# Performance work log

Hardware: AMD Instinct MI355X
Metric: run time of the kernel (lower is better)

The kernel has to match this reference:

```python
import jax, jax.numpy as jnp
import numpy as np

B, Q, K, D, H = 2, 1024, 4096, 1024, 16
DH = D // H
LN_EPS = 1e-5


def setup_inputs() -> dict:
    key = jax.random.key(0)
    ks = jax.random.split(key, 10)
    queries = jax.random.normal(ks[0], (B, Q, D), jnp.float32)
    keys = jax.random.normal(ks[1], (B, K, D), jnp.float32)
    values = jax.random.normal(ks[2], (B, K, D), jnp.float32)
    # 128 words of 8 query tokens each: boundaries 0,8,...,1024 (sorted, unique)
    word_boundaries = jnp.arange(0, Q + 1, 8, dtype=jnp.int32)  # [129]
    # monotone map from query positions to char/key positions in [0, K]
    char_boundaries = jnp.sort(jax.random.randint(ks[3], (Q,), 0, K + 1, dtype=jnp.int32))
    s = 0.02
    ln_gamma = jnp.ones((D,), jnp.float32)
    ln_beta = jnp.zeros((D,), jnp.float32)
    in_proj_w = jax.random.normal(ks[4], (3 * D, D), jnp.float32) * s
    in_proj_b = jnp.zeros((3 * D,), jnp.float32)
    out_w = jax.random.normal(ks[5], (D, D), jnp.float32) * s
    out_b = jnp.zeros((D,), jnp.float32)
    return dict(queries=queries, keys=keys, values=values,
                word_boundaries=word_boundaries, char_boundaries=char_boundaries,
                ln_gamma=ln_gamma, ln_beta=ln_beta,
                in_proj_w=in_proj_w, in_proj_b=in_proj_b,
                out_w=out_w, out_b=out_b)


def char_aware_mask(wb, cb, q_len, k_len):
    """Vectorized version of the per-word python loop.
    Float mask of 0/1 (PyTorch ADDS a float attn_mask to the scores)."""
    ws, we = wb[:-1], wb[1:]                     # word start/end in query coords [nW]
    nW = ws.shape[0]
    cs = cb[ws]                                  # char span start per word
    ce = cb[we - 1]                              # char span end per word
    q = jnp.arange(q_len)
    i = jnp.clip(jnp.searchsorted(wb, q, side='right') - 1, 0, nW - 1)  # word id per query row
    valid = (q >= ws[i]) & (q < we[i])           # rows actually written by the loop
    j = jnp.arange(k_len)[None, :]               # [1, K]
    in_char = (j >= cs[i][:, None]) & (j < ce[i][:, None])
    # prev word: keys [wb[i-1], wb[i]) (query-coord indices used on key axis, as in source)
    ps = ws[jnp.maximum(i - 1, 0)]
    in_prev = (i > 0)[:, None] & (j >= ps[:, None]) & (j < ws[i][:, None])
    # next word: keys [wb[i+1], wb[i+2])
    ns = we[i]
    ne = wb[jnp.minimum(i + 2, nW)]
    in_next = (i < nW - 1)[:, None] & (j >= ns[:, None]) & (j < ne[:, None])
    return (valid[:, None] & (in_char | in_prev | in_next)).astype(jnp.float32)


def reference(queries, keys, values, word_boundaries, char_boundaries,
              ln_gamma, ln_beta, in_proj_w, in_proj_b, out_w, out_b):
    b, q_len, d = queries.shape
    k_len = keys.shape[1]
    mask = char_aware_mask(word_boundaries, char_boundaries, q_len, k_len)  # [Q, K]
    # LayerNorm(queries)
    mu = jnp.mean(queries, axis=-1, keepdims=True)
    var = jnp.var(queries, axis=-1, keepdims=True)
    x = (queries - mu) * jax.lax.rsqrt(var + LN_EPS) * ln_gamma + ln_beta
    # MultiheadAttention(x, keys, values, attn_mask=mask) -- float mask added to logits
    wq, wk, wv = jnp.split(in_proj_w, 3, axis=0)
    bq, bk, bv = jnp.split(in_proj_b, 3)
    qh = (x @ wq.T + bq).reshape(b, q_len, H, DH)
    kh = (keys @ wk.T + bk).reshape(b, k_len, H, DH)
    vh = (values @ wv.T + bv).reshape(b, k_len, H, DH)
    scale = 1.0 / jnp.sqrt(jnp.asarray(DH, queries.dtype))
    scores = jnp.einsum('bqhd,bkhd->bhqk', qh * scale, kh) + mask[None, None]
    attn = jax.nn.softmax(scores, axis=-1)
    ctx = jnp.einsum('bhqk,bkhd->bqhd', attn, vh).reshape(b, q_len, d)
    out = ctx @ out_w.T + out_b
    # residual; dropout is identity at inference
    return queries + out
```

## Files before the change

### kernel.cpp

```cpp
#include <hip/hip_runtime.h>
#include <hip/hip_bf16.h>


typedef __attribute__((ext_vector_type(8))) short bf16x8;
typedef __attribute__((ext_vector_type(4))) float f32x4;
typedef __attribute__((ext_vector_type(16))) float f32x16;

#define L2E 1.44269504088896341f
#define CSCALE (0.125f * L2E)
#define NSPLIT 4

__device__ __forceinline__ short f2bf(float f) {
  __hip_bfloat16 h = __float2bfloat16(f);
  return reinterpret_cast<short&>(h);
}

__device__ __forceinline__ unsigned cvtpk(float a, float b) {
  unsigned r;
  asm("v_cvt_pk_bf16_f32 %0, %1, %2" : "=v"(r) : "v"(a), "v"(b));
  return r;
}

__device__ __forceinline__ float fexp2(float x) {
#if __has_builtin(__builtin_amdgcn_exp2f)
  return __builtin_amdgcn_exp2f(x);
#else
  float r;
  asm("v_exp_f32 %0, %1" : "=v"(r) : "v"(x));
  return r;
#endif
}

__device__ __forceinline__ void halfswap(unsigned a, unsigned b, unsigned& x, unsigned& y) {
#if __has_builtin(__builtin_amdgcn_permlane32_swap)
  auto r = __builtin_amdgcn_permlane32_swap(a, b, false, false);
  x = (unsigned)r[0];
  y = (unsigned)r[1];
#else
  unsigned ca = (unsigned)__shfl_xor((int)a, 32);
  unsigned cb = (unsigned)__shfl_xor((int)b, 32);
  bool h = ((threadIdx.x & 63) >> 5) != 0;
  x = h ? cb : a;
  y = h ? b : ca;
#endif
}

__device__ __forceinline__ void gload16(const void* g, void* l) {
  __builtin_amdgcn_global_load_lds(
      (const __attribute__((address_space(1))) void*)g,
      (__attribute__((address_space(3))) void*)l, 16, 0, 0);
}

template <int N>
__device__ __forceinline__ void phase_end() {
  __builtin_amdgcn_sched_barrier(0);
  if constexpr (N == 8)
    asm volatile("s_waitcnt vmcnt(8)" ::: "memory");
  else if constexpr (N == 6)
    asm volatile("s_waitcnt vmcnt(6)" ::: "memory");
  else if constexpr (N == 5)
    asm volatile("s_waitcnt vmcnt(5)" ::: "memory");
  else if constexpr (N == 4)
    asm volatile("s_waitcnt vmcnt(4)" ::: "memory");
  else if constexpr (N == 2)
    asm volatile("s_waitcnt vmcnt(2)" ::: "memory");
  else
    asm volatile("s_waitcnt vmcnt(0)" ::: "memory");
  __builtin_amdgcn_s_barrier();
  __builtin_amdgcn_sched_barrier(0);
}

__device__ __forceinline__ void wait_lgkm0() {
  __builtin_amdgcn_sched_barrier(0);
  asm volatile("s_waitcnt lgkmcnt(0)" ::: "memory");
  __builtin_amdgcn_sched_barrier(0);
}

__global__ __launch_bounds__(256) void prep_kernel(const float* __restrict__ w,
                                                   const float* __restrict__ o,
                                                   short* __restrict__ dw,
                                                   short* __restrict__ dof,
                                                   const float* __restrict__ x,
                                                   const float* __restrict__ gamma,
                                                   const float* __restrict__ beta,
                                                   short* __restrict__ xout,
                                                   const int* __restrict__ wb,
                                                   const int* __restrict__ cb,
                                                   int* __restrict__ iv,
                                                   const float* __restrict__ keys,
                                                   const float* __restrict__ values,
                                                   short* __restrict__ kbf,
                                                   short* __restrict__ vbf) {
  const int blk = blockIdx.x;
  const int t = threadIdx.x;
  if (blk < 4096) {
    long i = ((long)blk * 256 + t) * 4;
    const float* s;
    short* d;
    if (i < 3145728) { s = w + i; d = dw + i; }
    else { s = o + (i - 3145728); d = dof + (i - 3145728); }
    float4 xv = *(const float4*)s;
    uint2 r;
    r.x = cvtpk(xv.x, xv.y);
    r.y = cvtpk(xv.z, xv.w);
    *(uint2*)d = r;
  } else if (blk < 6144) {
    const int row = blk - 4096;
    float4 v = ((const float4*)(x + (size_t)row * 1024))[t];
    float s = v.x + v.y + v.z + v.w;
    float ss = v.x * v.x + v.y * v.y + v.z * v.z + v.w * v.w;
#pragma unroll
    for (int d = 32; d; d >>= 1) { s += __shfl_xor(s, d); ss += __shfl_xor(ss, d); }
    __shared__ float red[8];
    int wv2 = t >> 6, lane = t & 63;
    if (lane == 0) { red[wv2] = s; red[4 + wv2] = ss; }
    __syncthreads();
    s = red[0] + red[1] + red[2] + red[3];
    ss = red[4] + red[5] + red[6] + red[7];
    float mean = s * (1.0f / 1024.0f);
    float var = ss * (1.0f / 1024.0f) - mean * mean;
    float rstd = rsqrtf(var + 1e-5f);
    float4 g = ((const float4*)gamma)[t];
    float4 b = ((const float4*)beta)[t];
    uint2 oo;
    oo.x = cvtpk((v.x - mean) * rstd * g.x + b.x, (v.y - mean) * rstd * g.y + b.y);
    oo.y = cvtpk((v.z - mean) * rstd * g.z + b.z, (v.w - mean) * rstd * g.w + b.w);
    ((uint2*)(xout + (size_t)row * 1024))[t] = oo;
  } else if (blk < 6148) {
    int q = (blk - 6144) * 256 + t;
    if (q >= 1024) return;
    int cnt = 0;
    for (int k = 0; k < 129; ++k) cnt += (wb[k] <= q) ? 1 : 0;
    int i = cnt - 1;
    i = i < 0 ? 0 : (i > 127 ? 127 : i);
    bool valid = (q >= wb[i]) && (q < wb[i + 1]);
    int cs = 0, ce = 0, pl = 0, ph = 0, nl = 0, nh = 0;
    if (valid) {
      cs = cb[wb[i]];
      ce = cb[wb[i + 1] - 1];
      if (i > 0) { pl = wb[i - 1]; ph = wb[i]; }
      if (i < 127) { nl = wb[i + 1]; nh = wb[(i + 2 <= 128) ? i + 2 : 128]; }
    }
    int* p = iv + q * 8;
    p[0] = cs; p[1] = ce; p[2] = pl; p[3] = ph; p[4] = nl; p[5] = nh; p[6] = 0; p[7] = 0;
  } else {
    long i = ((long)(blk - 6148) * 256 + t) * 4;
    const float* s;
    short* d;
    if (i < 8388608) { s = keys + i; d = kbf + i; }
    else { s = values + (i - 8388608); d = vbf + (i - 8388608); }
    float4 xv = *(const float4*)s;
    uint2 r;
    r.x = cvtpk(xv.x, xv.y);
    r.y = cvtpk(xv.z, xv.w);
    *(uint2*)d = r;
  }
}

__device__ __forceinline__ unsigned inrange3(int key, const int* p) {
  bool m = (key >= p[0] && key < p[1]) || (key >= p[2] && key < p[3]) ||
           (key >= p[4] && key < p[5]);
  return m ? 1u : 0u;
}

__global__ __launch_bounds__(256) void mask_frag_kernel(const int* __restrict__ iv,
                                                        uint4* __restrict__ pmf) {
  int idx = blockIdx.x * 256 + threadIdx.x;
  int lane = idx & 63;
  int wg = (idx >> 6) & 31;
  int t = idx >> 11;
  int l31 = lane & 31, hi = lane >> 5;
  uint4 o = {0u, 0u, 0u, 0u};
  if (!hi) {
    int key0 = t * 64 + l31, key1 = key0 + 32;
    const int* p0 = iv + (wg * 32 + 0) * 8;
    const int* p1 = iv + (wg * 32 + 8) * 8;
    const int* p2 = iv + (wg * 32 + 16) * 8;
    const int* p3 = iv + (wg * 32 + 24) * 8;
    unsigned b0 = inrange3(key0, p0), b1 = inrange3(key0, p1);
    unsigned b2 = inrange3(key0, p2), b3 = inrange3(key0, p3);
    o.x = (b0 | (b1 << 16)) * 0x3F80u;
    o.y = (b2 | (b3 << 16)) * 0x3F80u;
    b0 = inrange3(key1, p0); b1 = inrange3(key1, p1);
    b2 = inrange3(key1, p2); b3 = inrange3(key1, p3);
    o.z = (b0 | (b1 << 16)) * 0x3F80u;
    o.w = (b2 | (b3 << 16)) * 0x3F80u;
  }
  pmf[idx] = o;
}

__device__ __forceinline__ void kv256_body(short* lds, const short* __restrict__ Agl,
                                           const short* __restrict__ Bgl,
                                           const float* __restrict__ bias,
                                           short* __restrict__ Cout, int mode,
                                           int bx, int by) {
  const int tid = (int)threadIdx.x;
  const int lane = tid & 63;
  const int w = tid >> 6;
  const int wm = w >> 2, wn = w & 3;
  const int l16 = lane & 15, lhi = lane >> 4;
  const int gc8 = (lane & 7) ^ (lane >> 3);
  const int lr = lane >> 3;
  const int rsw = (l16 & 7) << 4;
  const int m0 = bx * 256, n0 = by * 256;

  f32x4 acc[8][4];
#pragma unroll
  for (int i = 0; i < 8; ++i)
#pragma unroll
    for (int j = 0; j < 4; ++j) acc[i][j] = f32x4{0.f, 0.f, 0.f, 0.f};

  auto SU = [&](int k, int unit) {
    const int k0 = k * 64;
    short* base = lds + (k & 1) * 32768;
#pragma unroll
    for (int j = 0; j < 2; ++j) {
      int i = w * 2 + j;
      int ch;
      bool isA;
      if (unit == 1)      { ch = (i < 8) ? i : i + 8;       isA = true; }
      else if (unit == 4) { ch = 8 + ((i < 8) ? i : i + 8); isA = true; }
      else if (unit == 2) { ch = (i >> 2) * 8 + (i & 3);    isA = false; }
      else                { ch = 4 + (i >> 2) * 8 + (i & 3); isA = false; }
      const short* g = isA ? (Agl + (size_t)(m0 + ch * 8 + lr) * 1024 + k0 + gc8 * 8)
                           : (Bgl + (size_t)(n0 + ch * 8 + lr) * 1024 + k0 + gc8 * 8);
      gload16(g, base + (isA ? 0 : 16384) + ch * 512);
    }
  };

  bf16x8 af[4][2], b0[2][2], b1[2][2];
  auto LDA = [&](int bsel, int qm) {
    const char* cA = (const char*)(lds + bsel * 32768);
#pragma unroll
    for (int mt = 0; mt < 4; ++mt)
#pragma unroll
      for (int kk = 0; kk < 2; ++kk) {
        int row = wm * 128 + qm * 64 + mt * 16 + l16;
        af[mt][kk] = *(const bf16x8*)(cA + row * 128 + ((kk * 64 + lhi * 16) ^ rsw));
      }
  };
  auto LDB = [&](int bsel, int qn, bf16x8 (&bf)[2][2]) {
    const char* cB = (const char*)(lds + bsel * 32768) + 32768;
#pragma unroll
    for (int nt = 0; nt < 2; ++nt)
#pragma unroll
      for (int kk = 0; kk < 2; ++kk) {
        int row = wn * 64 + qn * 32 + nt * 16 + l16;
        bf[nt][kk] = *(const bf16x8*)(cB + row * 128 + ((kk * 64 + lhi * 16) ^ rsw));
      }
  };
  auto MM = [&](int qm, int qn, bf16x8 (&bf)[2][2]) {
    __builtin_amdgcn_s_setprio(1);
#pragma unroll
    for (int kk = 0; kk < 2; ++kk)
#pragma unroll
      for (int mt = 0; mt < 4; ++mt)
#pragma unroll
        for (int nt = 0; nt < 2; ++nt)
          acc[qm * 4 + mt][qn * 2 + nt] = __builtin_amdgcn_mfma_f32_16x16x32_bf16(
              af[mt][kk], bf[nt][kk], acc[qm * 4 + mt][qn * 2 + nt], 0, 0, 0);
    __builtin_amdgcn_s_setprio(0);
  };

  SU(0, 1); SU(0, 2); SU(0, 3); SU(0, 4);
  SU(1, 1); SU(1, 2);
  phase_end<8>();

#pragma unroll 2
  for (int k = 0; k < 14; ++k) {
    const int bs = k & 1;
    LDA(bs, 0); LDB(bs, 0, b0); SU(k + 1, 3);
    wait_lgkm0(); MM(0, 0, b0); phase_end<8>();
    LDB(bs, 1, b1); SU(k + 1, 4);
    wait_lgkm0(); MM(0, 1, b1); phase_end<8>();
    LDA(bs, 1); SU(k + 2, 1);
    wait_lgkm0(); MM(1, 0, b0); phase_end<8>();
    SU(k + 2, 2);
    MM(1, 1, b1); phase_end<8>();
  }
  {
    LDA(0, 0); LDB(0, 0, b0); SU(15, 3);
    wait_lgkm0(); MM(0, 0, b0); phase_end<8>();
    LDB(0, 1, b1); SU(15, 4);
    wait_lgkm0(); MM(0, 1, b1); phase_end<8>();
    LDA(0, 1);
    wait_lgkm0(); MM(1, 0, b0); phase_end<8>();
    MM(1, 1, b1); phase_end<4>();
  }
  {
    LDA(1, 0); LDB(1, 0, b0);
    wait_lgkm0(); MM(0, 0, b0); phase_end<2>();
    LDB(1, 1, b1);
    wait_lgkm0(); MM(0, 1, b1); phase_end<0>();
    LDA(1, 1);
    wait_lgkm0(); MM(1, 0, b0);
    MM(1, 1, b1);
  }

#pragma unroll
  for (int mt = 0; mt < 8; ++mt)
#pragma unroll
    for (int nt = 0; nt < 4; ++nt) {
      int n = n0 + wn * 64 + nt * 16 + l16;
#pragma unroll
      for (int r = 0; r < 4; ++r) {
        int m = m0 + wm * 128 + mt * 16 + lhi * 4 + r;
        float v = acc[mt][nt][r];
        if (mode == 0) {
          int bb = m >> 12, key = m & 4095;
          int hh = n >> 6, dhl = n & 63;
          Cout[((size_t)((bb * 16 + hh) * 4096 + key)) * 64 + dhl] = f2bf(v + bias[n]);
        } else {
          int bb = n >> 12, key = n & 4095;
          Cout[((size_t)(bb * 1024 + m)) * 4096 + key] = f2bf(v + bias[m]);
        }
      }
    }
}

__device__ __forceinline__ void gemmQO_body(short* lA, short* lB,
                                            const short* __restrict__ A,
                                            const short* __restrict__ W,
                                            const float* __restrict__ bias,
                                            const float* __restrict__ resid,
                                            void* __restrict__ Cout, int mode,
                                            float scale, int bxi, int byi) {
  const int lane = threadIdx.x & 63;
  const int w = threadIdx.x >> 6;
  const int m0 = bxi * 64;
  const int n0 = byi * 128;
  const int wm = w >> 2, wn = w & 3;
  const int l16 = lane & 15, lhi = lane >> 4;

  const int gc8 = (lane & 7) ^ (lane >> 3);
  const int lr = lane >> 3;
  const int rsw = (l16 & 7) << 4;

  f32x4 zero = {0.f, 0.f, 0.f, 0.f};
  f32x4 acc[2][2];
#pragma unroll
  for (int i = 0; i < 2; ++i)
#pragma unroll
    for (int j = 0; j < 2; ++j) acc[i][j] = zero;

  for (int k0 = 0; k0 < 1024; k0 += 64) {
    __syncthreads();
#pragma unroll
    for (int j = 0; j < 3; ++j) {
      int c = w * 3 + j;
      if (c < 8)
        gload16(A + (size_t)(m0 + c * 8 + lr) * 1024 + k0 + gc8 * 8, &lA[c * 512]);
      else
        gload16(W + (size_t)(n0 + (c - 8) * 8 + lr) * 1024 + k0 + gc8 * 8,
                &lB[(c - 8) * 512]);
    }
    __syncthreads();
    bf16x8 af[2][2], bfr[2][2];
#pragma unroll
    for (int mt = 0; mt < 2; ++mt)
#pragma unroll
      for (int kk = 0; kk < 2; ++kk)
        af[mt][kk] = *(const bf16x8*)((const char*)lA + (wm * 32 + mt * 16 + l16) * 128 +
                                      ((kk * 64 + lhi * 16) ^ rsw));
#pragma unroll
    for (int nt = 0; nt < 2; ++nt)
#pragma unroll
      for (int kk = 0; kk < 2; ++kk)
        bfr[nt][kk] = *(const bf16x8*)((const char*)lB + (wn * 32 + nt * 16 + l16) * 128 +
                                       ((kk * 64 + lhi * 16) ^ rsw));
#pragma unroll
    for (int kk = 0; kk < 2; ++kk)
#pragma unroll
      for (int mt = 0; mt < 2; ++mt)
#pragma unroll
        for (int nt = 0; nt < 2; ++nt)
          acc[mt][nt] = __builtin_amdgcn_mfma_f32_16x16x32_bf16(af[mt][kk], bfr[nt][kk],
                                                                acc[mt][nt], 0, 0, 0);
  }

#pragma unroll
  for (int mt = 0; mt < 2; ++mt)
#pragma unroll
    for (int nt = 0; nt < 2; ++nt) {
      int col = n0 + wn * 32 + nt * 16 + l16;
      float bs = bias[col];
#pragma unroll
      for (int r = 0; r < 4; ++r) {
        int row = m0 + wm * 32 + mt * 16 + lhi * 4 + r;
        float v = acc[mt][nt][r] + bs;
        if (mode == 0) {
          ((short*)Cout)[(size_t)row * 1024 + col] = f2bf(v * scale);
        } else {
          size_t idx = (size_t)row * 1024 + col;
          ((float*)Cout)[idx] = v + resid[idx];
        }
      }
    }
}

__global__ __launch_bounds__(512, 2) void megaGemm_kernel(const short* __restrict__ kbf,
                                                          const short* __restrict__ wk,
                                                          const float* __restrict__ kbias,
                                                          const short* __restrict__ wv,
                                                          const short* __restrict__ vbf,
                                                          const float* __restrict__ vbias,
                                                          short* __restrict__ khp,
                                                          short* __restrict__ vhT,
                                                          const short* __restrict__ xb,
                                                          const short* __restrict__ wq,
                                                          const float* __restrict__ qbias,
                                                          short* __restrict__ qhb) {
  __shared__ __attribute__((aligned(16))) short lds[65536];
  int id = blockIdx.x;
  if (id < 128) {
    kv256_body(lds, kbf, wk, kbias, khp, 0, id & 31, id >> 5);
  } else if (id < 256) {
    int i2 = id & 127;
    kv256_body(lds, wv, vbf, vbias, vhT, 1, i2 >> 5, i2 & 31);
  } else {
    int i2 = id - 256;
    gemmQO_body(lds, lds + 4096, xb, wq, qbias, nullptr, qhb, 0, CSCALE, i2 & 31, i2 >> 5);
  }
}

__global__ __launch_bounds__(512, 4) void gemmQO_kernel(const short* __restrict__ A,
                                                        const short* __restrict__ W,
                                                        const float* __restrict__ bias,
                                                        const float* __restrict__ resid,
                                                        void* __restrict__ Cout, int mode,
                                                        float scale) {
  __shared__ __attribute__((aligned(16))) short lA[4096];
  __shared__ __attribute__((aligned(16))) short lB[8192];
  gemmQO_body(lA, lB, A, W, bias, resid, Cout, mode, scale, blockIdx.x, blockIdx.y);
}

__global__ __launch_bounds__(256) void attn11_kernel(const short* __restrict__ qh,
                                                     const short* __restrict__ khp,
                                                     const short* __restrict__ vtp,
                                                     const uint4* __restrict__ pmf,
                                                     short* __restrict__ pacc,
                                                     float* __restrict__ pml) {
  const int tid = threadIdx.x;
  const int lane = tid & 63;
  const int w = tid >> 6;
  const int l31 = lane & 31;
  const int hi = lane >> 5;
  const int id = blockIdx.x;
  const int qb = id >> 7;
  const int g = id & 127;
  const int bh = g >> 2;
  const int ks = g & 3;
  const int b = bh >> 4, h = bh & 15;

  __shared__ __attribute__((aligned(16))) short sK[2][4096];
  __shared__ __attribute__((aligned(16))) short sV[2][4096];

  const int wq0 = qb * 128 + w * 32;
  const int qrow = wq0 + l31;
  bf16x8 qf0, qf1, qf2, qf3;
  {
    const short* qp = qh + ((size_t)(b * 1024 + qrow)) * 1024 + h * 64 + hi * 8;
    qf0 = *(const bf16x8*)(qp);
    qf1 = *(const bf16x8*)(qp + 16);
    qf2 = *(const bf16x8*)(qp + 32);
    qf3 = *(const bf16x8*)(qp + 48);
  }

  bf16x8 bmv;
  {
    union { unsigned u[4]; bf16x8 v; } t;
    t.u[0] = t.u[1] = t.u[2] = t.u[3] = 0;
    int lj = l31 >> 3;
    unsigned val = 0x3FB9u << (16 * (lj & 1));
    if (!hi) t.u[lj >> 1] = val;
    bmv = t.v;
  }

  f32x16 fzero;
#pragma unroll
  for (int i = 0; i < 16; ++i) fzero[i] = 0.f;

  const int kchunk = ks * 1024;
  const int sub = (lane & 7) ^ (lane >> 3);
  const int r8 = lane >> 3;
  const size_t kbase_g = ((size_t)bh * 4096 + kchunk) * 64;
  const size_t vbase_g = ((size_t)bh * 64) * 4096 + (size_t)kchunk;
  const uint4* pmfp = pmf + ((size_t)(ks * 16) * 32 + qb * 4 + w) * 64 + lane;

  f32x16 acc0, acc1;
#pragma unroll
  for (int i = 0; i < 16; ++i) { acc0[i] = 0.f; acc1[i] = 0.f; }
  float rs = 0.f;

  const int koff_swz = (lane & 7) << 4;

  auto STAGE = [&](int buf, int t) {
    int kt = t * 64;
#pragma unroll
    for (int q2 = 0; q2 < 2; ++q2) {
      int ch = w * 2 + q2;
      gload16(khp + kbase_g + (size_t)(kt + ch * 8 + r8) * 64 + sub * 8,
              (short*)sK[buf] + ch * 512);
      gload16(vtp + vbase_g + (size_t)(ch * 8 + r8) * 4096 + kt + sub * 8,
              (short*)sV[buf] + ch * 512);
    }
  };

  auto HALF = [&](int buf, unsigned mlo, unsigned mhi, int rowb, bf16x8& paA, bf16x8& paB) {
    bf16x8 am;
    {
      union { unsigned u[4]; bf16x8 v; } f;
      f.u[0] = mlo; f.u[1] = mhi; f.u[2] = 0; f.u[3] = 0;
      am = f.v;
    }
    __builtin_amdgcn_s_setprio(1);
    f32x16 ss = __builtin_amdgcn_mfma_f32_32x32x16_bf16(am, bmv, fzero, 0, 0, 0);
#pragma unroll
    for (int c = 0; c < 4; ++c) {
      int off = (c * 32 + hi * 16) ^ koff_swz;
      bf16x8 k0 = *(const bf16x8*)((const char*)sK[buf] + (rowb + l31) * 128 + off);
      bf16x8 qc = (c == 0) ? qf0 : (c == 1) ? qf1 : (c == 2) ? qf2 : qf3;
      ss = __builtin_amdgcn_mfma_f32_32x32x16_bf16(k0, qc, ss, 0, 0, 0);
    }
    __builtin_amdgcn_s_setprio(0);
#pragma unroll
    for (int r = 0; r < 16; ++r) ss[r] = fexp2(ss[r]);
    {
      float t0 = ss[0] + ss[1], t1 = ss[2] + ss[3], t2 = ss[4] + ss[5], t3 = ss[6] + ss[7];
      float t4 = ss[8] + ss[9], t5 = ss[10] + ss[11], t6 = ss[12] + ss[13],
            t7 = ss[14] + ss[15];
      rs += ((t0 + t1) + (t2 + t3)) + ((t4 + t5) + (t6 + t7));
    }
    unsigned a01 = cvtpk(ss[0], ss[1]), a23 = cvtpk(ss[2], ss[3]);
    unsigned a45 = cvtpk(ss[4], ss[5]), a67 = cvtpk(ss[6], ss[7]);
    unsigned a89 = cvtpk(ss[8], ss[9]), aAB = cvtpk(ss[10], ss[11]);
    unsigned aCD = cvtpk(ss[12], ss[13]), aEF = cvtpk(ss[14], ss[15]);
    union { unsigned u[4]; bf16x8 v; } f;
    halfswap(a01, a45, f.u[0], f.u[2]);
    halfswap(a23, a67, f.u[1], f.u[3]);
    paA = f.v;
    halfswap(a89, aCD, f.u[0], f.u[2]);
    halfswap(aAB, aEF, f.u[1], f.u[3]);
    paB = f.v;
  };

  uint4 mf_cur = pmfp[0];
  uint4 mf_next = mf_cur;
  STAGE(0, 0);
  __syncthreads();
  int buf = 0;

  for (int t = 0; t < 16; ++t) {
    if (t < 15) {
      STAGE(buf ^ 1, t + 1);
      mf_next = pmfp[(size_t)(t + 1) * 2048];
    }

    bf16x8 pa0, pa1, pa2, pa3;
    HALF(buf, mf_cur.x, mf_cur.y, 0, pa0, pa1);
    HALF(buf, mf_cur.z, mf_cur.w, 32, pa2, pa3);

    __builtin_amdgcn_s_setprio(1);
#pragma unroll
    for (int kb16 = 0; kb16 < 4; ++kb16) {
      int off = (kb16 * 32 + hi * 16) ^ koff_swz;
      bf16x8 v0 = *(const bf16x8*)((const char*)sV[buf] + l31 * 128 + off);
      bf16x8 v1 = *(const bf16x8*)((const char*)sV[buf] + (32 + l31) * 128 + off);
      bf16x8 pa = (kb16 == 0) ? pa0 : (kb16 == 1) ? pa1 : (kb16 == 2) ? pa2 : pa3;
      acc0 = __builtin_amdgcn_mfma_f32_32x32x16_bf16(pa, v0, acc0, 0, 0, 0);
      acc1 = __builtin_amdgcn_mfma_f32_32x32x16_bf16(pa, v1, acc1, 0, 0, 0);
    }
    __builtin_amdgcn_s_setprio(0);
    __syncthreads();
    buf ^= 1;
    mf_cur = mf_next;
  }

  short* paccp = pacc + (((size_t)ks * 32 + bh) * 1024) * 64;
#pragma unroll
  for (int r = 0; r < 16; r += 2) {
    int q0 = wq0 + ((r & 3) + 8 * (r >> 2)) + 4 * hi;
    int q1 = wq0 + (((r + 1) & 3) + 8 * ((r + 1) >> 2)) + 4 * hi;
    unsigned u0 = cvtpk(acc0[r], acc0[r + 1]);
    unsigned u1 = cvtpk(acc1[r], acc1[r + 1]);
    paccp[(size_t)q0 * 64 + l31] = (short)(u0 & 0xffffu);
    paccp[(size_t)q1 * 64 + l31] = (short)(u0 >> 16);
    paccp[(size_t)q0 * 64 + 32 + l31] = (short)(u1 & 0xffffu);
    paccp[(size_t)q1 * 64 + 32 + l31] = (short)(u1 >> 16);
  }
  rs += __shfl_xor(rs, 32);
  if (hi == 0) {
    float* mlp = pml + ((size_t)ks * 32 + bh) * 1024;
    mlp[wq0 + l31] = rs;
  }
}

__global__ __launch_bounds__(256) void combine_kernel(const short* __restrict__ pacc,
                                                      const float* __restrict__ pml,
                                                      short* __restrict__ ctx) {
  int idx = blockIdx.x * 256 + threadIdx.x;
  int dh4 = idx & 15;
  int row = idx >> 4;
  int bh = row >> 10, q = row & 1023;
  float L = 0.f, o0 = 0.f, o1 = 0.f, o2 = 0.f, o3 = 0.f;
#pragma unroll
  for (int k = 0; k < NSPLIT; ++k) {
    L += pml[((size_t)k * 32 + bh) * 1024 + q];
    uint2 u = *(const uint2*)&pacc[(((size_t)k * 32 + bh) * 1024 + q) * 64 + dh4 * 4];
    unsigned a = u.x, b2 = u.y;
    unsigned t0 = a << 16, t1 = a & 0xffff0000u, t2 = b2 << 16, t3 = b2 & 0xffff0000u;
    o0 += reinterpret_cast<float&>(t0);
    o1 += reinterpret_cast<float&>(t1);
    o2 += reinterpret_cast<float&>(t2);
    o3 += reinterpret_cast<float&>(t3);
  }
  float inv = 1.0f / L;
  uint2 st;
  st.x = cvtpk(o0 * inv, o1 * inv);
  st.y = cvtpk(o2 * inv, o3 * inv);
  int b = bh >> 4, h = bh & 15;
  *(uint2*)&ctx[((size_t)(b * 1024 + q)) * 1024 + h * 64 + dh4 * 4] = st;
}

extern "C" void kernel_launch(void* const* d_in, const int* in_sizes, int n_in,
                              void* d_out, int out_size, void* d_ws, size_t ws_size,
                              hipStream_t stream) {
  const float* queries = (const float*)d_in[0];
  const float* keys    = (const float*)d_in[1];
  const float* values  = (const float*)d_in[2];
  const int*   wb      = (const int*)d_in[3];
  const int*   cb      = (const int*)d_in[4];
  const float* gamma   = (const float*)d_in[5];
  const float* beta    = (const float*)d_in[6];
  const float* ipw     = (const float*)d_in[7];
  const float* ipb     = (const float*)d_in[8];
  const float* ow      = (const float*)d_in[9];
  const float* ob      = (const float*)d_in[10];
  float* out = (float*)d_out;

  char* p = (char*)d_ws;
  short* xb  = (short*)p; p += (size_t)2048 * 1024 * 2;
  short* kb  = (short*)p; p += (size_t)8192 * 1024 * 2;
  short* vb  = (short*)p; p += (size_t)8192 * 1024 * 2;
  short* wpb = (short*)p; p += (size_t)3072 * 1024 * 2;
  short* owb = (short*)p; p += (size_t)1024 * 1024 * 2;
  short* qhb = (short*)p; p += (size_t)2048 * 1024 * 2;
  short* khp = (short*)p; p += (size_t)8192 * 1024 * 2;
  short* vhT = (short*)p; p += (size_t)8192 * 1024 * 2;
  short* ctx = (short*)p; p += (size_t)2048 * 1024 * 2;
  int* iv = (int*)p; p += (size_t)1024 * 8 * 4;
  uint4* pmf = (uint4*)p; p += (size_t)64 * 32 * 64 * 16;
  if ((size_t)(p - (char*)d_ws) > ws_size) return;

  short* pacc = kb;
  float* pml  = (float*)wpb;

  prep_kernel<<<22532, 256, 0, stream>>>(ipw, ow, wpb, owb, queries, gamma, beta, xb,
                                         wb, cb, iv, keys, values, kb, vb);
  mask_frag_kernel<<<512, 256, 0, stream>>>(iv, pmf);

  megaGemm_kernel<<<512, 512, 0, stream>>>(kb, wpb + 1048576, ipb + 1024,
                                           wpb + 2097152, vb, ipb + 2048,
                                           khp, vhT, xb, wpb, ipb, qhb);

  attn11_kernel<<<1024, 256, 0, stream>>>(qhb, khp, vhT, pmf, pacc, pml);
  combine_kernel<<<2048, 256, 0, stream>>>(pacc, pml, ctx);

  gemmQO_kernel<<<dim3(32, 8), 512, 0, stream>>>(ctx, owb, ob, queries, out, 2, 1.f);
}
```

Baseline: 153.8 us.

## Process 64 query rows per wave in attention to reuse K/V tiles

Each wave in the attention kernel now computes two 32-row query blocks against the same K and V LDS fragments instead of one. That halves the number of blocks and halves the K/V global-to-LDS staging and LDS reads per query row. In exchange, each wave holds twice the accumulators and Q fragments, which raises VGPR pressure and can lower occupancy. With only 512 blocks there is also less parallelism to hide latency.

Result: slower. 164.1 us (+6.7%).

```diff
diff --git a/kernel.cpp b/kernel.cpp
--- a/kernel.cpp
+++ b/kernel.cpp
@@ -434,7 +434,7 @@
   gemmQO_body(lA, lB, A, W, bias, resid, Cout, mode, scale, blockIdx.x, blockIdx.y);
 }
 
-__global__ __launch_bounds__(256) void attn11_kernel(const short* __restrict__ qh,
+__global__ __launch_bounds__(256) void attn12_kernel(const short* __restrict__ qh,
                                                      const short* __restrict__ khp,
                                                      const short* __restrict__ vtp,
                                                      const uint4* __restrict__ pmf,
@@ -455,15 +455,19 @@
   __shared__ __attribute__((aligned(16))) short sK[2][4096];
   __shared__ __attribute__((aligned(16))) short sV[2][4096];
 
-  const int wq0 = qb * 128 + w * 32;
-  const int qrow = wq0 + l31;
-  bf16x8 qf0, qf1, qf2, qf3;
+  const int wq0 = qb * 256 + w * 64;
+  bf16x8 qA0, qA1, qA2, qA3, qB0, qB1, qB2, qB3;
   {
-    const short* qp = qh + ((size_t)(b * 1024 + qrow)) * 1024 + h * 64 + hi * 8;
-    qf0 = *(const bf16x8*)(qp);
-    qf1 = *(const bf16x8*)(qp + 16);
-    qf2 = *(const bf16x8*)(qp + 32);
-    qf3 = *(const bf16x8*)(qp + 48);
+    const short* qpA = qh + ((size_t)(b * 1024 + wq0 + l31)) * 1024 + h * 64 + hi * 8;
+    qA0 = *(const bf16x8*)(qpA);
+    qA1 = *(const bf16x8*)(qpA + 16);
+    qA2 = *(const bf16x8*)(qpA + 32);
+    qA3 = *(const bf16x8*)(qpA + 48);
+    const short* qpB = qpA + (size_t)32 * 1024;
+    qB0 = *(const bf16x8*)(qpB);
+    qB1 = *(const bf16x8*)(qpB + 16);
+    qB2 = *(const bf16x8*)(qpB + 32);
+    qB3 = *(const bf16x8*)(qpB + 48);
   }
 
   bf16x8 bmv;
@@ -485,12 +489,15 @@
   const int r8 = lane >> 3;
   const size_t kbase_g = ((size_t)bh * 4096 + kchunk) * 64;
   const size_t vbase_g = ((size_t)bh * 64) * 4096 + (size_t)kchunk;
-  const uint4* pmfp = pmf + ((size_t)(ks * 16) * 32 + qb * 4 + w) * 64 + lane;
-
-  f32x16 acc0, acc1;
-#pragma unroll
-  for (int i = 0; i < 16; ++i) { acc0[i] = 0.f; acc1[i] = 0.f; }
-  float rs = 0.f;
+  const uint4* pmfA = pmf + ((size_t)(ks * 16)) * 2048 + (size_t)(qb * 8 + w * 2) * 64 + lane;
+  const uint4* pmfB = pmfA + 64;
+
+  f32x16 accA0, accA1, accB0, accB1;
+#pragma unroll
+  for (int i = 0; i < 16; ++i) {
+    accA0[i] = 0.f; accA1[i] = 0.f; accB0[i] = 0.f; accB1[i] = 0.f;
+  }
+  float rsA = 0.f, rsB = 0.f;
 
   const int koff_swz = (lane & 7) << 4;
 
@@ -506,46 +513,71 @@
     }
   };
 
-  auto HALF = [&](int buf, unsigned mlo, unsigned mhi, int rowb, bf16x8& paA, bf16x8& paB) {
-    bf16x8 am;
+  auto HALF2 = [&](int buf, unsigned mAlo, unsigned mAhi, unsigned mBlo, unsigned mBhi,
+                   int rowb, bf16x8& pA0, bf16x8& pA1, bf16x8& pB0, bf16x8& pB1) {
+    bf16x8 amA, amB;
     {
       union { unsigned u[4]; bf16x8 v; } f;
-      f.u[0] = mlo; f.u[1] = mhi; f.u[2] = 0; f.u[3] = 0;
-      am = f.v;
+      f.u[0] = mAlo; f.u[1] = mAhi; f.u[2] = 0; f.u[3] = 0;
+      amA = f.v;
+      f.u[0] = mBlo; f.u[1] = mBhi;
+      amB = f.v;
     }
     __builtin_amdgcn_s_setprio(1);
-    f32x16 ss = __builtin_amdgcn_mfma_f32_32x32x16_bf16(am, bmv, fzero, 0, 0, 0);
+    f32x16 ssA = __builtin_amdgcn_mfma_f32_32x32x16_bf16(amA, bmv, fzero, 0, 0, 0);
+    f32x16 ssB = __builtin_amdgcn_mfma_f32_32x32x16_bf16(amB, bmv, fzero, 0, 0, 0);
 #pragma unroll
     for (int c = 0; c < 4; ++c) {
       int off = (c * 32 + hi * 16) ^ koff_swz;
       bf16x8 k0 = *(const bf16x8*)((const char*)sK[buf] + (rowb + l31) * 128 + off);
-      bf16x8 qc = (c == 0) ? qf0 : (c == 1) ? qf1 : (c == 2) ? qf2 : qf3;
-      ss = __builtin_amdgcn_mfma_f32_32x32x16_bf16(k0, qc, ss, 0, 0, 0);
+      bf16x8 qa = (c == 0) ? qA0 : (c == 1) ? qA1 : (c == 2) ? qA2 : qA3;
+      bf16x8 qb2 = (c == 0) ? qB0 : (c == 1) ? qB1 : (c == 2) ? qB2 : qB3;
+      ssA = __builtin_amdgcn_mfma_f32_32x32x16_bf16(k0, qa, ssA, 0, 0, 0);
+      ssB = __builtin_amdgcn_mfma_f32_32x32x16_bf16(k0, qb2, ssB, 0, 0, 0);
     }
     __builtin_amdgcn_s_setprio(0);
 #pragma unroll
-    for (int r = 0; r < 16; ++r) ss[r] = fexp2(ss[r]);
+    for (int r = 0; r < 16; ++r) { ssA[r] = fexp2(ssA[r]); ssB[r] = fexp2(ssB[r]); }
     {
-      float t0 = ss[0] + ss[1], t1 = ss[2] + ss[3], t2 = ss[4] + ss[5], t3 = ss[6] + ss[7];
-      float t4 = ss[8] + ss[9], t5 = ss[10] + ss[11], t6 = ss[12] + ss[13],
-            t7 = ss[14] + ss[15];
-      rs += ((t0 + t1) + (t2 + t3)) + ((t4 + t5) + (t6 + t7));
-    }
-    unsigned a01 = cvtpk(ss[0], ss[1]), a23 = cvtpk(ss[2], ss[3]);
-    unsigned a45 = cvtpk(ss[4], ss[5]), a67 = cvtpk(ss[6], ss[7]);
-    unsigned a89 = cvtpk(ss[8], ss[9]), aAB = cvtpk(ss[10], ss[11]);
-    unsigned aCD = cvtpk(ss[12], ss[13]), aEF = cvtpk(ss[14], ss[15]);
-    union { unsigned u[4]; bf16x8 v; } f;
-    halfswap(a01, a45, f.u[0], f.u[2]);
-    halfswap(a23, a67, f.u[1], f.u[3]);
-    paA = f.v;
-    halfswap(a89, aCD, f.u[0], f.u[2]);
-    halfswap(aAB, aEF, f.u[1], f.u[3]);
-    paB = f.v;
+      float t0 = ssA[0] + ssA[1], t1 = ssA[2] + ssA[3], t2 = ssA[4] + ssA[5],
+            t3 = ssA[6] + ssA[7], t4 = ssA[8] + ssA[9], t5 = ssA[10] + ssA[11],
+            t6 = ssA[12] + ssA[13], t7 = ssA[14] + ssA[15];
+      rsA += ((t0 + t1) + (t2 + t3)) + ((t4 + t5) + (t6 + t7));
+      float u0 = ssB[0] + ssB[1], u1 = ssB[2] + ssB[3], u2 = ssB[4] + ssB[5],
+            u3 = ssB[6] + ssB[7], u4 = ssB[8] + ssB[9], u5 = ssB[10] + ssB[11],
+            u6 = ssB[12] + ssB[13], u7 = ssB[14] + ssB[15];
+      rsB += ((u0 + u1) + (u2 + u3)) + ((u4 + u5) + (u6 + u7));
+    }
+    {
+      unsigned a01 = cvtpk(ssA[0], ssA[1]), a23 = cvtpk(ssA[2], ssA[3]);
+      unsigned a45 = cvtpk(ssA[4], ssA[5]), a67 = cvtpk(ssA[6], ssA[7]);
+      unsigned a89 = cvtpk(ssA[8], ssA[9]), aAB = cvtpk(ssA[10], ssA[11]);
+      unsigned aCD = cvtpk(ssA[12], ssA[13]), aEF = cvtpk(ssA[14], ssA[15]);
+      union { unsigned u[4]; bf16x8 v; } f;
+      halfswap(a01, a45, f.u[0], f.u[2]);
+      halfswap(a23, a67, f.u[1], f.u[3]);
+      pA0 = f.v;
+      halfswap(a89, aCD, f.u[0], f.u[2]);
+      halfswap(aAB, aEF, f.u[1], f.u[3]);
+      pA1 = f.v;
+    }
+    {
+      unsigned a01 = cvtpk(ssB[0], ssB[1]), a23 = cvtpk(ssB[2], ssB[3]);
+      unsigned a45 = cvtpk(ssB[4], ssB[5]), a67 = cvtpk(ssB[6], ssB[7]);
+      unsigned a89 = cvtpk(ssB[8], ssB[9]), aAB = cvtpk(ssB[10], ssB[11]);
+      unsigned aCD = cvtpk(ssB[12], ssB[13]), aEF = cvtpk(ssB[14], ssB[15]);
+      union { unsigned u[4]; bf16x8 v; } f;
+      halfswap(a01, a45, f.u[0], f.u[2]);
+      halfswap(a23, a67, f.u[1], f.u[3]);
+      pB0 = f.v;
+      halfswap(a89, aCD, f.u[0], f.u[2]);
+      halfswap(aAB, aEF, f.u[1], f.u[3]);
+      pB1 = f.v;
+    }
   };
 
-  uint4 mf_cur = pmfp[0];
-  uint4 mf_next = mf_cur;
+  uint4 mfA_cur = pmfA[0], mfB_cur = pmfB[0];
+  uint4 mfA_next = mfA_cur, mfB_next = mfB_cur;
   STAGE(0, 0);
   __syncthreads();
   int buf = 0;
@@ -553,12 +585,13 @@
   for (int t = 0; t < 16; ++t) {
     if (t < 15) {
       STAGE(buf ^ 1, t + 1);
-      mf_next = pmfp[(size_t)(t + 1) * 2048];
-    }
-
-    bf16x8 pa0, pa1, pa2, pa3;
-    HALF(buf, mf_cur.x, mf_cur.y, 0, pa0, pa1);
-    HALF(buf, mf_cur.z, mf_cur.w, 32, pa2, pa3);
+      mfA_next = pmfA[(size_t)(t + 1) * 2048];
+      mfB_next = pmfB[(size_t)(t + 1) * 2048];
+    }
+
+    bf16x8 pA0, pA1, pA2, pA3, pB0, pB1, pB2, pB3;
+    HALF2(buf, mfA_cur.x, mfA_cur.y, mfB_cur.x, mfB_cur.y, 0, pA0, pA1, pB0, pB1);
+    HALF2(buf, mfA_cur.z, mfA_cur.w, mfB_cur.z, mfB_cur.w, 32, pA2, pA3, pB2, pB3);
 
     __builtin_amdgcn_s_setprio(1);
 #pragma unroll
@@ -566,32 +599,50 @@
       int off = (kb16 * 32 + hi * 16) ^ koff_swz;
       bf16x8 v0 = *(const bf16x8*)((const char*)sV[buf] + l31 * 128 + off);
       bf16x8 v1 = *(const bf16x8*)((const char*)sV[buf] + (32 + l31) * 128 + off);
-      bf16x8 pa = (kb16 == 0) ? pa0 : (kb16 == 1) ? pa1 : (kb16 == 2) ? pa2 : pa3;
-      acc0 = __builtin_amdgcn_mfma_f32_32x32x16_bf16(pa, v0, acc0, 0, 0, 0);
-      acc1 = __builtin_amdgcn_mfma_f32_32x32x16_bf16(pa, v1, acc1, 0, 0, 0);
+      bf16x8 pa = (kb16 == 0) ? pA0 : (kb16 == 1) ? pA1 : (kb16 == 2) ? pA2 : pA3;
+      bf16x8 pb = (kb16 == 0) ? pB0 : (kb16 == 1) ? pB1 : (kb16 == 2) ? pB2 : pB3;
+      accA0 = __builtin_amdgcn_mfma_f32_32x32x16_bf16(pa, v0, accA0, 0, 0, 0);
+      accA1 = __builtin_amdgcn_mfma_f32_32x32x16_bf16(pa, v1, accA1, 0, 0, 0);
+      accB0 = __builtin_amdgcn_mfma_f32_32x32x16_bf16(pb, v0, accB0, 0, 0, 0);
+      accB1 = __builtin_amdgcn_mfma_f32_32x32x16_bf16(pb, v1, accB1, 0, 0, 0);
     }
     __builtin_amdgcn_s_setprio(0);
     __syncthreads();
     buf ^= 1;
-    mf_cur = mf_next;
+    mfA_cur = mfA_next;
+    mfB_cur = mfB_next;
   }
 
   short* paccp = pacc + (((size_t)ks * 32 + bh) * 1024) * 64;
 #pragma unroll
   for (int r = 0; r < 16; r += 2) {
-    int q0 = wq0 + ((r & 3) + 8 * (r >> 2)) + 4 * hi;
-    int q1 = wq0 + (((r + 1) & 3) + 8 * ((r + 1) >> 2)) + 4 * hi;
-    unsigned u0 = cvtpk(acc0[r], acc0[r + 1]);
-    unsigned u1 = cvtpk(acc1[r], acc1[r + 1]);
-    paccp[(size_t)q0 * 64 + l31] = (short)(u0 & 0xffffu);
-    paccp[(size_t)q1 * 64 + l31] = (short)(u0 >> 16);
-    paccp[(size_t)q0 * 64 + 32 + l31] = (short)(u1 & 0xffffu);
-    paccp[(size_t)q1 * 64 + 32 + l31] = (short)(u1 >> 16);
-  }
-  rs += __shfl_xor(rs, 32);
+    int d0 = ((r & 3) + 8 * (r >> 2)) + 4 * hi;
+    int d1 = (((r + 1) & 3) + 8 * ((r + 1) >> 2)) + 4 * hi;
+    {
+      int q0 = wq0 + d0, q1 = wq0 + d1;
+      unsigned u0 = cvtpk(accA0[r], accA0[r + 1]);
+      unsigned u1 = cvtpk(accA1[r], accA1[r + 1]);
+      paccp[(size_t)q0 * 64 + l31] = (short)(u0 & 0xffffu);
+      paccp[(size_t)q1 * 64 + l31] = (short)(u0 >> 16);
+      paccp[(size_t)q0 * 64 + 32 + l31] = (short)(u1 & 0xffffu);
+      paccp[(size_t)q1 * 64 + 32 + l31] = (short)(u1 >> 16);
+    }
+    {
+      int q0 = wq0 + 32 + d0, q1 = wq0 + 32 + d1;
+      unsigned u0 = cvtpk(accB0[r], accB0[r + 1]);
+      unsigned u1 = cvtpk(accB1[r], accB1[r + 1]);
+      paccp[(size_t)q0 * 64 + l31] = (short)(u0 & 0xffffu);
+      paccp[(size_t)q1 * 64 + l31] = (short)(u0 >> 16);
+      paccp[(size_t)q0 * 64 + 32 + l31] = (short)(u1 & 0xffffu);
+      paccp[(size_t)q1 * 64 + 32 + l31] = (short)(u1 >> 16);
+    }
+  }
+  rsA += __shfl_xor(rsA, 32);
+  rsB += __shfl_xor(rsB, 32);
   if (hi == 0) {
     float* mlp = pml + ((size_t)ks * 32 + bh) * 1024;
-    mlp[wq0 + l31] = rs;
+    mlp[wq0 + l31] = rsA;
+    mlp[wq0 + 32 + l31] = rsB;
   }
 }
 
@@ -663,7 +714,7 @@
                                            wpb + 2097152, vb, ipb + 2048,
                                            khp, vhT, xb, wpb, ipb, qhb);
 
-  attn11_kernel<<<1024, 256, 0, stream>>>(qhb, khp, vhT, pmf, pacc, pml);
+  attn12_kernel<<<512, 256, 0, stream>>>(qhb, khp, vhT, pmf, pacc, pml);
   combine_kernel<<<2048, 256, 0, stream>>>(pacc, pml, ctx);
 
   gemmQO_kernel<<<dim3(32, 8), 512, 0, stream>>>(ctx, owb, ob, queries, out, 2, 1.f);
```

## Coarsen fp32-to-bf16 conversion blocks and relax megaGemm vmcnt waits per k-step

Applied to the files above, without the earlier changes.

The prep kernel's cast path now has each of 2048 blocks convert ten float4 chunks in a grid-stride loop across weights, out-proj, keys and values, replacing about 20k single-chunk blocks. This cuts block launch overhead and lets each thread keep several loads in flight. In megaGemm, the per-phase global-load waits plus barriers become plain LDS barriers, with one vmcnt(4) wait per k-iteration instead. That deepens the asynchronous load pipeline, but correctness now depends on the stage buffers not being read before their loads land.

New measurement: 153.8 us. Within noise of the previous version (-0.0%).

```diff
diff --git a/kernel.cpp b/kernel.cpp
--- a/kernel.cpp
+++ b/kernel.cpp
@@ -56,14 +56,10 @@
   __builtin_amdgcn_sched_barrier(0);
   if constexpr (N == 8)
     asm volatile("s_waitcnt vmcnt(8)" ::: "memory");
-  else if constexpr (N == 6)
-    asm volatile("s_waitcnt vmcnt(6)" ::: "memory");
   else if constexpr (N == 5)
     asm volatile("s_waitcnt vmcnt(5)" ::: "memory");
   else if constexpr (N == 4)
     asm volatile("s_waitcnt vmcnt(4)" ::: "memory");
-  else if constexpr (N == 2)
-    asm volatile("s_waitcnt vmcnt(2)" ::: "memory");
   else
     asm volatile("s_waitcnt vmcnt(0)" ::: "memory");
   __builtin_amdgcn_s_barrier();
@@ -73,6 +69,12 @@
 __device__ __forceinline__ void wait_lgkm0() {
   __builtin_amdgcn_sched_barrier(0);
   asm volatile("s_waitcnt lgkmcnt(0)" ::: "memory");
+  __builtin_amdgcn_sched_barrier(0);
+}
+
+__device__ __forceinline__ void lds_barrier() {
+  __builtin_amdgcn_sched_barrier(0);
+  __builtin_amdgcn_s_barrier();
   __builtin_amdgcn_sched_barrier(0);
 }
 
@@ -93,19 +95,34 @@
                                                    short* __restrict__ vbf) {
   const int blk = blockIdx.x;
   const int t = threadIdx.x;
-  if (blk < 4096) {
-    long i = ((long)blk * 256 + t) * 4;
-    const float* s;
-    short* d;
-    if (i < 3145728) { s = w + i; d = dw + i; }
-    else { s = o + (i - 3145728); d = dof + (i - 3145728); }
-    float4 xv = *(const float4*)s;
-    uint2 r;
-    r.x = cvtpk(xv.x, xv.y);
-    r.y = cvtpk(xv.z, xv.w);
-    *(uint2*)d = r;
-  } else if (blk < 6144) {
-    const int row = blk - 4096;
+  if (blk < 2048) {
+    int base = blk * 256 + t;
+#pragma unroll
+    for (int i = 0; i < 10; ++i) {
+      long f = (long)base + (long)i * 524288;
+      const float* s;
+      short* d;
+      if (f < 786432) {
+        long e = f * 4;
+        s = w + e; d = dw + e;
+      } else if (f < 1048576) {
+        long e = (f - 786432) * 4;
+        s = o + e; d = dof + e;
+      } else if (f < 3145728) {
+        long e = (f - 1048576) * 4;
+        s = keys + e; d = kbf + e;
+      } else {
+        long e = (f - 3145728) * 4;
+        s = values + e; d = vbf + e;
+      }
+      float4 xv = *(const float4*)s;
+      uint2 r;
+      r.x = cvtpk(xv.x, xv.y);
+      r.y = cvtpk(xv.z, xv.w);
+      *(uint2*)d = r;
+    }
+  } else if (blk < 4096) {
+    const int row = blk - 2048;
     float4 v = ((const float4*)(x + (size_t)row * 1024))[t];
     float s = v.x + v.y + v.z + v.w;
     float ss = v.x * v.x + v.y * v.y + v.z * v.z + v.w * v.w;
@@ -126,8 +143,8 @@
     oo.x = cvtpk((v.x - mean) * rstd * g.x + b.x, (v.y - mean) * rstd * g.y + b.y);
     oo.y = cvtpk((v.z - mean) * rstd * g.z + b.z, (v.w - mean) * rstd * g.w + b.w);
     ((uint2*)(xout + (size_t)row * 1024))[t] = oo;
-  } else if (blk < 6148) {
-    int q = (blk - 6144) * 256 + t;
+  } else {
+    int q = (blk - 4096) * 256 + t;
     if (q >= 1024) return;
     int cnt = 0;
     for (int k = 0; k < 129; ++k) cnt += (wb[k] <= q) ? 1 : 0;
@@ -143,17 +160,6 @@
     }
     int* p = iv + q * 8;
     p[0] = cs; p[1] = ce; p[2] = pl; p[3] = ph; p[4] = nl; p[5] = nh; p[6] = 0; p[7] = 0;
-  } else {
-    long i = ((long)(blk - 6148) * 256 + t) * 4;
-    const float* s;
-    short* d;
-    if (i < 8388608) { s = keys + i; d = kbf + i; }
-    else { s = values + (i - 8388608); d = vbf + (i - 8388608); }
-    float4 xv = *(const float4*)s;
-    uint2 r;
-    r.x = cvtpk(xv.x, xv.y);
-    r.y = cvtpk(xv.z, xv.w);
-    *(uint2*)d = r;
   }
 }
 
@@ -264,34 +270,36 @@
 
   SU(0, 1); SU(0, 2); SU(0, 3); SU(0, 4);
   SU(1, 1); SU(1, 2);
-  phase_end<8>();
+  phase_end<4>();
 
 #pragma unroll 2
   for (int k = 0; k < 14; ++k) {
     const int bs = k & 1;
     LDA(bs, 0); LDB(bs, 0, b0); SU(k + 1, 3);
-    wait_lgkm0(); MM(0, 0, b0); phase_end<8>();
+    wait_lgkm0(); MM(0, 0, b0); lds_barrier();
     LDB(bs, 1, b1); SU(k + 1, 4);
-    wait_lgkm0(); MM(0, 1, b1); phase_end<8>();
+    wait_lgkm0(); MM(0, 1, b1); lds_barrier();
     LDA(bs, 1); SU(k + 2, 1);
-    wait_lgkm0(); MM(1, 0, b0); phase_end<8>();
+    wait_lgkm0(); MM(1, 0, b0); lds_barrier();
     SU(k + 2, 2);
-    MM(1, 1, b1); phase_end<8>();
+    MM(1, 1, b1);
+    phase_end<4>();
   }
   {
     LDA(0, 0); LDB(0, 0, b0); SU(15, 3);
-    wait_lgkm0(); MM(0, 0, b0); phase_end<8>();
+    wait_lgkm0(); MM(0, 0, b0); lds_barrier();
     LDB(0, 1, b1); SU(15, 4);
-    wait_lgkm0(); MM(0, 1, b1); phase_end<8>();
+    wait_lgkm0(); MM(0, 1, b1); lds_barrier();
     LDA(0, 1);
-    wait_lgkm0(); MM(1, 0, b0); phase_end<8>();
-    MM(1, 1, b1); phase_end<4>();
+    wait_lgkm0(); MM(1, 0, b0); lds_barrier();
+    MM(1, 1, b1);
+    phase_end<0>();
   }
   {
     LDA(1, 0); LDB(1, 0, b0);
-    wait_lgkm0(); MM(0, 0, b0); phase_end<2>();
+    wait_lgkm0(); MM(0, 0, b0);
     LDB(1, 1, b1);
-    wait_lgkm0(); MM(0, 1, b1); phase_end<0>();
+    wait_lgkm0(); MM(0, 1, b1);
     LDA(1, 1);
     wait_lgkm0(); MM(1, 0, b0);
     MM(1, 1, b1);
@@ -655,8 +663,8 @@
   short* pacc = kb;
   float* pml  = (float*)wpb;
 
-  prep_kernel<<<22532, 256, 0, stream>>>(ipw, ow, wpb, owb, queries, gamma, beta, xb,
-                                         wb, cb, iv, keys, values, kb, vb);
+  prep_kernel<<<4100, 256, 0, stream>>>(ipw, ow, wpb, owb, queries, gamma, beta, xb,
+                                        wb, cb, iv, keys, values, kb, vb);
   mask_frag_kernel<<<512, 256, 0, stream>>>(iv, pmf);
 
   megaGemm_kernel<<<512, 512, 0, stream>>>(kb, wpb + 1048576, ipb + 1024,
```
